# Kernel tuning notes

Hardware: AMD Instinct MI355X
Metric: run time of the kernel (lower is better)

Reference implementation:

```python
import jax, jax.numpy as jnp
import numpy as np
import math

INPUT_SIZE = 1024
OUTPUT_SIZE = 1024
N_HEADS = 8
N_EXPERTS = 16
PROJ = INPUT_SIZE // N_HEADS  # 128


def sinusoidal_pos_embedding(d_model, max_len, pos_offset):
    # positions pos_offset .. pos_offset+max_len-1, standard sin/cos interleave
    position = (jnp.arange(max_len, dtype=jnp.float32) + pos_offset)[:, None]
    div_term = jnp.exp(jnp.arange(0, d_model, 2, dtype=jnp.float32) * (-math.log(10000.0) / d_model))
    pe = jnp.zeros((max_len, d_model), dtype=jnp.float32)
    pe = pe.at[:, 0::2].set(jnp.sin(position * div_term))
    pe = pe.at[:, 1::2].set(jnp.cos(position * div_term))
    return pe


def shift(posmat):
    # Transformer-XL style relative shift: [..., n_out, 2*n_in-1] -> [..., n_out, n_in]
    n_in = (posmat.shape[-1] + 1) // 2
    n_neg = n_in - 1
    n_out = posmat.shape[-2]
    x = posmat.reshape(posmat.shape[:-2] + (-1,))
    x = x[..., 1:1 + n_out * (n_in + n_neg - 1)]
    x = x.reshape(x.shape[:-1] + (n_out, n_in + n_neg - 1))
    return x[..., n_neg - 1:]


def setup_inputs() -> dict:
    key = jax.random.key(0)
    ks = jax.random.split(key, 8)
    B, S = 4, 1024
    std_in = math.sqrt(1.0 / INPUT_SIZE)
    std_out = math.sqrt(1.0 / (N_HEADS * PROJ))
    std_pos = math.sqrt(1.0 / INPUT_SIZE)
    return {
        "curr_state": jax.random.normal(ks[0], (B, S, INPUT_SIZE), jnp.float32),
        "attend_to": jax.random.normal(ks[1], (B, S, INPUT_SIZE), jnp.float32),
        "data_to_q": jax.random.normal(ks[2], (N_EXPERTS, INPUT_SIZE, PROJ), jnp.float32) * std_in,
        "data_to_kv": jax.random.normal(ks[3], (INPUT_SIZE, 2 * PROJ), jnp.float32) * std_in,
        "out_proj": jax.random.normal(ks[4], (N_EXPERTS, PROJ, OUTPUT_SIZE), jnp.float32) * std_out,
        "pos_to_pk": jax.random.normal(ks[5], (PROJ, INPUT_SIZE), jnp.float32) * std_pos,
        "sel_dst": jax.random.normal(ks[6], (N_EXPERTS, INPUT_SIZE), jnp.float32) * std_in,
        "scale": jnp.full((1,), 1.0 / math.sqrt(PROJ), jnp.float32),
    }


def reference(curr_state, attend_to, data_to_q, data_to_kv, out_proj, pos_to_pk, sel_dst, scale):
    B, S, _ = curr_state.shape
    # --- expert selection (mode='my', sigmoid, eval: no expert dropout) ---
    sel = jnp.einsum('bsi,ei->bse', curr_state, sel_dst)           # gate logits
    sel_top, sel_index = jax.lax.top_k(sel, N_HEADS)               # [B,S,H]
    sel_val = jax.nn.sigmoid(sel_top)                              # [B,S,H]
    sc = jnp.sqrt(scale)                                           # scale applied to q, k, k_pos
    # --- relative position keys ---
    pemb = sinusoidal_pos_embedding(INPUT_SIZE, 2 * S - 1, -(S - 1))
    k_pos = (pemb @ pos_to_pk.T) * sc                              # [2S-1, P]
    # --- shared K/V ---
    kv = attend_to @ data_to_kv                                    # [B,S,2P]
    k = kv[..., :PROJ] * sc
    v = kv[..., PROJ:]
    # --- expert-selected Q (dense over experts, then gather selected) ---
    q_all = jnp.einsum('bsi,eip->bsep', curr_state, data_to_q) * sc  # [B,S,E,P]
    q = jnp.take_along_axis(q_all, sel_index[..., None], axis=2)     # [B,S,H,P]
    q = q.transpose(0, 2, 1, 3)                                      # [B,H,S,P]
    # --- attention with relative position shift (mask=None path) ---
    att = shift(jnp.einsum('bhsp,tp->bhst', q, k_pos)) + jnp.einsum('bhsp,btp->bhst', q, k)
    att = jax.nn.softmax(att, axis=-1)                               # [B,H,S,S]
    res = jnp.einsum('bhst,btp->bhsp', att, v)                       # [B,H,S,P]
    # --- expert-selected, sigmoid-gated output projection, summed over heads ---
    g = sel_val[..., None] * jax.nn.one_hot(sel_index, N_EXPERTS, dtype=res.dtype)  # [B,S,H,E]
    z = jnp.einsum('bshe,bhsp->bsep', g, res)                        # [B,S,E,P]
    out = jnp.einsum('bsep,epo->bso', z, out_proj)                   # [B,S,O]
    return out
```

## Files before the change

### kernel.cpp

```cpp
#include <hip/hip_runtime.h>
#include <math.h>


typedef __attribute__((ext_vector_type(8))) short short8;
typedef __attribute__((ext_vector_type(4))) float floatx4;

__device__ __forceinline__ float bf2f(unsigned int u) {
    union { unsigned int i; float f; } x; x.i = (u & 0xffffu) << 16; return x.f;
}
__device__ __forceinline__ unsigned short f2bf(float f) {
    union { float f; unsigned int i; } x; x.f = f;
    unsigned int r = x.i + 0x7fffu + ((x.i >> 16) & 1u);
    return (unsigned short)(r >> 16);
}

__device__ __forceinline__ void gload16(const void* g, void* l) {
    __builtin_amdgcn_global_load_lds(
        (const __attribute__((address_space(1))) unsigned int*)(uintptr_t)g,
        (__attribute__((address_space(3))) unsigned int*)(uintptr_t)l,
        16, 0, 0);
}


__global__ __launch_bounds__(256) void k_prep(const float* __restrict__ curr,
                                              const float* __restrict__ attend,
                                              const float* __restrict__ w_q,
                                              const float* __restrict__ w_out,
                                              const float* __restrict__ w_kv,
                                              const float* __restrict__ pos_pk,
                                              const float* __restrict__ sel_dst,
                                              float* __restrict__ selval,
                                              int* __restrict__ selidx,
                                              unsigned short* __restrict__ afrag,
                                              unsigned short* __restrict__ attfrag,
                                              unsigned short* __restrict__ bfragq,
                                              unsigned short* __restrict__ bfragw,
                                              unsigned short* __restrict__ bfragkv,
                                              unsigned short* __restrict__ bfragp,
                                              unsigned short* __restrict__ pefrag) {
    __shared__ float row[1024];
    __shared__ float sel[16];
    const int bx = blockIdx.x;
    const int t = threadIdx.x;

    if (bx < 2048) {
        const unsigned u = (unsigned)bx * 256 + t;
        const int half = u & 1;
        const int nlow = (u >> 1) & 15;
        const int koct = (u >> 5) & 3;
        const int kc   = (u >> 7) & 31;
        const int nt   = (u >> 12) & 127;
        const int n = nt * 16 + nlow;
        const int e = n >> 7, p = n & 127;
        const int k0 = kc * 32 + koct * 8 + half * 4;
        const float* src = w_q + (size_t)e * 131072 + (size_t)k0 * 128 + p;
        uint2 o;
        o.x = (unsigned)f2bf(src[0])   | ((unsigned)f2bf(src[128]) << 16);
        o.y = (unsigned)f2bf(src[256]) | ((unsigned)f2bf(src[384]) << 16);
        const size_t chunk = ((size_t)nt * 32 + kc) * 64 + koct * 16 + nlow;
        *(uint2*)(bfragq + chunk * 8 + half * 4) = o;
    } else if (bx < 4096) {
        const unsigned u = (unsigned)(bx - 2048) * 256 + t;
        const int half = u & 1;
        const int nlow = (u >> 1) & 15;
        const int koct = (u >> 5) & 3;
        const int kc   = (u >> 7) & 63;
        const int nt   = (u >> 13) & 63;
        const int n = nt * 16 + nlow;
        const int k0 = kc * 32 + koct * 8 + half * 4;
        const float* src = w_out + (size_t)k0 * 1024 + n;
        uint2 o;
        o.x = (unsigned)f2bf(src[0])    | ((unsigned)f2bf(src[1024]) << 16);
        o.y = (unsigned)f2bf(src[2048]) | ((unsigned)f2bf(src[3072]) << 16);
        const size_t chunk = ((size_t)nt * 64 + kc) * 64 + koct * 16 + nlow;
        *(uint2*)(bfragw + chunk * 8 + half * 4) = o;
    } else if (bx < 4352) {
        const unsigned u = (unsigned)(bx - 4096) * 256 + t;
        const int half = u & 1;
        const int nlow = (u >> 1) & 15;
        const int koct = (u >> 5) & 3;
        const int kc   = (u >> 7) & 31;
        const int nt   = (u >> 12) & 15;
        const int n = nt * 16 + nlow;
        const int k0 = kc * 32 + koct * 8 + half * 4;
        const float* src = w_kv + (size_t)k0 * 256 + n;
        uint2 o;
        o.x = (unsigned)f2bf(src[0])   | ((unsigned)f2bf(src[256]) << 16);
        o.y = (unsigned)f2bf(src[512]) | ((unsigned)f2bf(src[768]) << 16);
        const size_t chunk = ((size_t)nt * 32 + kc) * 64 + koct * 16 + nlow;
        *(uint2*)(bfragkv + chunk * 8 + half * 4) = o;
    } else if (bx < 4480) {
        const int n = bx - 4352;
        float v[4];
#pragma unroll
        for (int d = 0; d < 4; ++d) v[d] = pos_pk[(size_t)n * 1024 + 4 * t + d];
        const int nt = n >> 4, kc = t >> 3;
        const int lane = ((t & 7) >> 1) * 16 + (n & 15);
        const size_t off = (((size_t)nt * 32 + kc) * 64 + lane) * 8 + 4 * (t & 1);
        uint2 o;
        o.x = (unsigned)f2bf(v[0]) | ((unsigned)f2bf(v[1]) << 16);
        o.y = (unsigned)f2bf(v[2]) | ((unsigned)f2bf(v[3]) << 16);
        *(uint2*)(bfragp + off) = o;
    } else if (bx < 6528) {
        const unsigned u = (unsigned)(bx - 4480) * 256 + t;
        const int half = u & 1;
        const int mlow = (u >> 1) & 15;
        const int koct = (u >> 5) & 3;
        const int kc   = (u >> 7) & 31;
        const int mt   = (u >> 12) & 127;
        const int m = mt * 16 + mlow;
        const int k0 = kc * 32 + koct * 8 + half * 4;
        uint2 o;
        if (m >= 2047) {
            o.x = 0u; o.y = 0u;
        } else {
            const float c1 = -logf(10000.f) / 1024.f;
            const float pos = (float)(m - 1023);
            const float a0 = pos * expf((float)k0 * c1);
            const float a1 = pos * expf((float)(k0 + 2) * c1);
            o.x = (unsigned)f2bf(sinf(a0)) | ((unsigned)f2bf(cosf(a0)) << 16);
            o.y = (unsigned)f2bf(sinf(a1)) | ((unsigned)f2bf(cosf(a1)) << 16);
        }
        const size_t chunk = ((size_t)mt * 32 + kc) * 64 + koct * 16 + mlow;
        *(uint2*)(pefrag + chunk * 8 + half * 4) = o;
    } else if (bx < 10624) {
        const int token = bx - 6528;
        const float4 v = ((const float4*)(curr + (size_t)token * 1024))[t];
        ((float4*)row)[t] = v;
        __syncthreads();
        const int wv = t >> 6, lane = t & 63;
        for (int e0 = 0; e0 < 4; ++e0) {
            const int e = wv * 4 + e0;
            const float* w = sel_dst + e * 1024;
            float p = 0.f;
            for (int i = lane; i < 1024; i += 64) p += row[i] * w[i];
            for (int off = 32; off; off >>= 1) p += __shfl_down(p, off, 64);
            if (lane == 0) sel[e] = p;
        }
        __syncthreads();
        if (t == 0) {
            float v16[16];
#pragma unroll
            for (int e = 0; e < 16; ++e) v16[e] = sel[e];
#pragma unroll
            for (int r = 0; r < 8; ++r) {
                int bi = 0; float bv = v16[0];
#pragma unroll
                for (int e = 1; e < 16; ++e) { if (v16[e] > bv) { bv = v16[e]; bi = e; } }
                selidx[token * 8 + r] = bi;
                selval[token * 8 + r] = 1.f / (1.f + __expf(-bv));
                v16[bi] = -INFINITY;
            }
        }
    } else if (bx < 14720) {
        const unsigned u = (unsigned)(bx - 10624) * 256 + t;
        const int half = u & 1;
        const int mlow = (u >> 1) & 15;
        const int koct = (u >> 5) & 3;
        const int kc   = (u >> 7) & 31;
        const int mt   = (u >> 12) & 255;
        const int m = mt * 16 + mlow;
        const int k0 = kc * 32 + koct * 8 + half * 4;
        const float4 v = *(const float4*)(curr + (size_t)m * 1024 + k0);
        uint2 o;
        o.x = (unsigned)f2bf(v.x) | ((unsigned)f2bf(v.y) << 16);
        o.y = (unsigned)f2bf(v.z) | ((unsigned)f2bf(v.w) << 16);
        const size_t chunk = ((size_t)mt * 32 + kc) * 64 + koct * 16 + mlow;
        *(uint2*)(afrag + chunk * 8 + half * 4) = o;
    } else {
        const unsigned u = (unsigned)(bx - 14720) * 256 + t;
        const int half = u & 1;
        const int mlow = (u >> 1) & 15;
        const int koct = (u >> 5) & 3;
        const int kc   = (u >> 7) & 31;
        const int mt   = (u >> 12) & 255;
        const int m = mt * 16 + mlow;
        const int k0 = kc * 32 + koct * 8 + half * 4;
        const float4 v = *(const float4*)(attend + (size_t)m * 1024 + k0);
        uint2 o;
        o.x = (unsigned)f2bf(v.x) | ((unsigned)f2bf(v.y) << 16);
        o.y = (unsigned)f2bf(v.z) | ((unsigned)f2bf(v.w) << 16);
        const size_t chunk = ((size_t)mt * 32 + kc) * 64 + koct * 16 + mlow;
        *(uint2*)(attfrag + chunk * 8 + half * 4) = o;
    }
}

__device__ __forceinline__ void gemm_core64(const unsigned short* __restrict__ Afrag,
                                            const unsigned short* __restrict__ Bfrag,
                                            int mt0, int nt0, int KC,
                                            unsigned short (*aT)[512],
                                            unsigned short (*bT)[512],
                                            floatx4 acc[4][2]) {
    const int t = threadIdx.x;
    const int w = t >> 6, lane = t & 63;
    const int wm = w >> 1, wn = w & 1;
    for (int kc = 0; kc < KC; ++kc) {
        __syncthreads();
        {
            const int fi = w * 3;
#pragma unroll
            for (int l = 0; l < 3; ++l) {
                const int f = fi + l;
                if (f < 8)
                    gload16(Afrag + (((size_t)(mt0 + f) * KC + kc) * 64 + lane) * 8, &aT[f][0]);
                else
                    gload16(Bfrag + (((size_t)(nt0 + f - 8) * KC + kc) * 64 + lane) * 8, &bT[f - 8][0]);
            }
        }
        __syncthreads();
        short8 af[4], bf[2];
#pragma unroll
        for (int i = 0; i < 4; ++i) af[i] = *(const short8*)&aT[wm * 4 + i][lane * 8];
#pragma unroll
        for (int j = 0; j < 2; ++j) bf[j] = *(const short8*)&bT[wn * 2 + j][lane * 8];
#pragma unroll
        for (int i = 0; i < 4; ++i)
#pragma unroll
            for (int j = 0; j < 2; ++j)
                acc[i][j] = __builtin_amdgcn_mfma_f32_16x16x32_bf16(af[i], bf[j], acc[i][j], 0, 0, 0);
    }
}

__global__ __launch_bounds__(256) void k_gemm3(const unsigned short* __restrict__ afrag,
                                               const unsigned short* __restrict__ bfragq,
                                               const unsigned short* __restrict__ attfrag,
                                               const unsigned short* __restrict__ bfragkv,
                                               const unsigned short* __restrict__ pefrag,
                                               const unsigned short* __restrict__ bfragp,
                                               const float* __restrict__ scale,
                                               unsigned short* __restrict__ qall,
                                               unsigned short* __restrict__ kfragg,
                                               unsigned short* __restrict__ vfragg,
                                               unsigned short* __restrict__ kposfg) {
    __shared__ __align__(16) unsigned short aT[8][512], bT[4][512];
    floatx4 acc[4][2];
#pragma unroll
    for (int i = 0; i < 4; ++i) { acc[i][0] = (floatx4){0,0,0,0}; acc[i][1] = (floatx4){0,0,0,0}; }
    const int bx = blockIdx.x;
    const int t = threadIdx.x, w = t >> 6, lane = t & 63;
    const int wm = w >> 1, wn = w & 1, lq = lane >> 4, lm = lane & 15;
    const float sc = sqrtf(scale[0]);

    if (bx < 1024) {
        const int gx = bx & 31, gy = bx >> 5;
        gemm_core64(afrag, bfragq, gx * 8, gy * 4, 32, aT, bT, acc);
#pragma unroll
        for (int i = 0; i < 4; ++i)
#pragma unroll
            for (int j = 0; j < 2; ++j)
#pragma unroll
                for (int r = 0; r < 4; ++r)
                    qall[(size_t)(gx * 128 + (wm * 4 + i) * 16 + lq * 4 + r) * 2048 +
                         gy * 64 + (wn * 2 + j) * 16 + lm] = f2bf(acc[i][j][r] * sc);
    } else if (bx < 1152) {
        const int q = bx - 1024;
        const int gx = q & 31, gy = q >> 5;
        gemm_core64(attfrag, bfragkv, gx * 8, gy * 4, 32, aT, bT, acc);
#pragma unroll
        for (int i = 0; i < 4; ++i)
#pragma unroll
            for (int j = 0; j < 2; ++j) {
                const int n = gy * 64 + (wn * 2 + j) * 16 + lm;
#pragma unroll
                for (int r = 0; r < 4; ++r) {
                    const int tok = gx * 128 + (wm * 4 + i) * 16 + lq * 4 + r;
                    const int bb = tok >> 10, jj = tok & 1023;
                    if (n < 128) {
                        const int p = n;
                        const size_t addr = ((((size_t)bb * 64 + (jj >> 4)) * 4 + (p >> 5)) * 64 +
                                             ((p & 31) >> 3) * 16 + (jj & 15)) * 8 + (p & 7);
                        kfragg[addr] = f2bf(acc[i][j][r] * sc);
                    } else {
                        const int p = n - 128;
                        const size_t addr = ((((size_t)bb * 32 + (jj >> 5)) * 8 + (p >> 4)) * 64 +
                                             ((jj & 31) >> 3) * 16 + (p & 15)) * 8 + (jj & 7);
                        vfragg[addr] = f2bf(acc[i][j][r]);
                    }
                }
            }
    } else {
        const int q = bx - 1152;
        const int gx = q & 15, gy = q >> 4;
        gemm_core64(pefrag, bfragp, gx * 8, gy * 4, 32, aT, bT, acc);
#pragma unroll
        for (int i = 0; i < 4; ++i)
#pragma unroll
            for (int j = 0; j < 2; ++j) {
                const int p = gy * 64 + (wn * 2 + j) * 16 + lm;
#pragma unroll
                for (int r = 0; r < 4; ++r) {
                    const int tp = gx * 128 + (wm * 4 + i) * 16 + lq * 4 + r;
                    const size_t addr = (((size_t)(tp >> 4) * 4 + (p >> 5)) * 64 +
                                         ((p & 31) >> 3) * 16 + (tp & 15)) * 8 + (p & 7);
                    kposfg[addr] = f2bf(acc[i][j][r] * sc);
                }
            }
    }
}

__global__ __launch_bounds__(256) void k_gemm_out(const unsigned short* __restrict__ Afrag,
                                                  const unsigned short* __restrict__ Bfrag,
                                                  float* __restrict__ out) {
    __shared__ __align__(16) unsigned short aT[8][512], bT[4][512];
    floatx4 acc[4][2];
#pragma unroll
    for (int i = 0; i < 4; ++i) { acc[i][0] = (floatx4){0,0,0,0}; acc[i][1] = (floatx4){0,0,0,0}; }
    gemm_core64(Afrag, Bfrag, blockIdx.x * 8, blockIdx.y * 4, 64, aT, bT, acc);
    const int t = threadIdx.x, w = t >> 6, lane = t & 63;
    const int wm = w >> 1, wn = w & 1, lq = lane >> 4, lm = lane & 15;
#pragma unroll
    for (int i = 0; i < 4; ++i)
#pragma unroll
        for (int j = 0; j < 2; ++j)
#pragma unroll
            for (int r = 0; r < 4; ++r)
                out[(size_t)(blockIdx.x * 128 + (wm * 4 + i) * 16 + lq * 4 + r) * 1024 +
                    blockIdx.y * 64 + (wn * 2 + j) * 16 + lm] = acc[i][j][r];
}

#define ATTN_FM 8.0f

__global__ __launch_bounds__(256, 2) void k_attn(const unsigned short* __restrict__ qall,
                                                 const unsigned short* __restrict__ kfragg,
                                                 const unsigned short* __restrict__ vfragg,
                                                 const unsigned short* __restrict__ kposfg,
                                                 const int* __restrict__ selidx,
                                                 const float* __restrict__ selval,
                                                 unsigned short* __restrict__ zfrag) {
    __shared__ __align__(16) union {
        struct {
            unsigned short pl[2][4][16][56];
            unsigned short kst[2][2][8][512];
            unsigned short vst[2][2][8][512];
        } s;
        float cmb[2][64][37];
    } sh;

    const int t = threadIdx.x;
    const int w = t >> 6, lane = t & 63;
    const int st = blockIdx.x & 63;
    const int hg = (blockIdx.x >> 6) & 3;
    const int b = blockIdx.x >> 8;
    const int wh = w & 1;
    const int ws = w >> 1;
    const int h = hg * 2 + wh;
    const int s0 = st * 16;
    const int lq = lane >> 4;
    const int lm = lane & 15;
    const int loff = lane * 16;

    short8 qf[4];
    {
        const int token = b * 1024 + s0 + lm;
        const int e = selidx[token * 8 + h];
        const unsigned short* qb = qall + (size_t)token * 2048 + e * 128 + lq * 8;
#pragma unroll
        for (int c = 0; c < 4; ++c) qf[c] = *(const short8*)(qb + c * 32);
    }
    short8 onesf;
#pragma unroll
    for (int i = 0; i < 8; ++i) onesf[i] = (short)0x3F80;

    int baddr[4], bsel[4];
#pragma unroll
    for (int r = 0; r < 4; ++r) {
        const int c0 = 15 + lm - (lq * 4 + r);
        baddr[r] = (lq * 16 + (c0 & 15)) * 4;
        bsel[r] = (c0 < 16) ? 1 : 0;
    }

    floatx4 acc[8], accl;
#pragma unroll
    for (int nt = 0; nt < 8; ++nt) acc[nt] = (floatx4){0.f, 0.f, 0.f, 0.f};
    accl = (floatx4){0.f, 0.f, 0.f, 0.f};

    const size_t koff = (size_t)ws * 131072;
    const char* pk = (const char*)kfragg + (size_t)b * 262144 + koff;
    const char* pv = (const char*)vfragg + (size_t)b * 262144 + koff;
    const char* pp = (const char*)kposfg + (size_t)((1008 - s0) >> 4) * 4096 + koff;

    if (wh == 0) {
#pragma unroll
        for (int q = 0; q < 8; ++q)
            gload16(pk + q * 1024 + loff, &sh.s.kst[0][ws][q][0]);
    } else {
#pragma unroll
        for (int q = 0; q < 8; ++q)
            gload16(pv + q * 1024 + loff, &sh.s.vst[0][ws][q][0]);
    }
    short8 n1c[4], n2c[4];
    floatx4 sp_carry = {0.f, 0.f, 0.f, 0.f};
    {
        short8 cry[4];
#pragma unroll
        for (int c = 0; c < 4; ++c) {
            cry[c] = *(const short8*)(pp + c * 1024 + loff);
            n1c[c] = *(const short8*)(pp + 4096 + c * 1024 + loff);
            n2c[c] = *(const short8*)(pp + 8192 + c * 1024 + loff);
        }
#pragma unroll
        for (int c = 0; c < 4; ++c)
            sp_carry = __builtin_amdgcn_mfma_f32_16x16x32_bf16(qf[c], cry[c], sp_carry, 0, 0, 0);
    }
    __syncthreads();

    unsigned short* pl0 = &sh.s.pl[0][w][0][0];
    unsigned short* pl1 = &sh.s.pl[1][w][0][0];

    for (int it = 0; it < 16; ++it) {
        const int cur = it & 1, nxt = cur ^ 1;
        if (it < 15) {
            if (wh == 0) {
#pragma unroll
                for (int q = 0; q < 8; ++q)
                    gload16(pk + 8192 + q * 1024 + loff, &sh.s.kst[nxt][ws][q][0]);
            } else {
#pragma unroll
                for (int q = 0; q < 8; ++q)
                    gload16(pv + 8192 + q * 1024 + loff, &sh.s.vst[nxt][ws][q][0]);
            }
        }
        short8 n1n[4], n2n[4];
        if (it < 15) {
#pragma unroll
            for (int c = 0; c < 4; ++c) {
                n1n[c] = *(const short8*)(pp + 12288 + c * 1024 + loff);
                n2n[c] = *(const short8*)(pp + 16384 + c * 1024 + loff);
            }
        }
        const floatx4 sp0 = sp_carry;
        floatx4 sp1 = {0.f, 0.f, 0.f, 0.f}, sp2 = {0.f, 0.f, 0.f, 0.f};
#pragma unroll
        for (int c = 0; c < 4; ++c) {
            sp1 = __builtin_amdgcn_mfma_f32_16x16x32_bf16(qf[c], n1c[c], sp1, 0, 0, 0);
            sp2 = __builtin_amdgcn_mfma_f32_16x16x32_bf16(qf[c], n2c[c], sp2, 0, 0, 0);
        }
        floatx4 sk0 = {0.f, 0.f, 0.f, 0.f}, sk1 = {0.f, 0.f, 0.f, 0.f};
#pragma unroll
        for (int c = 0; c < 4; ++c) {
            const short8 k0 = *(const short8*)&sh.s.kst[cur][ws][c][lane * 8];
            const short8 k1 = *(const short8*)&sh.s.kst[cur][ws][4 + c][lane * 8];
            sk0 = __builtin_amdgcn_mfma_f32_16x16x32_bf16(qf[c], k0, sk0, 0, 0, 0);
            sk1 = __builtin_amdgcn_mfma_f32_16x16x32_bf16(qf[c], k1, sk1, 0, 0, 0);
        }
        unsigned short* pl = cur ? pl1 : pl0;
#pragma unroll
        for (int r = 0; r < 4; ++r) {
            const int a = baddr[r];
            const float b0 = __int_as_float(__builtin_amdgcn_ds_bpermute(a, __float_as_int(sp0[r])));
            const float b1 = __int_as_float(__builtin_amdgcn_ds_bpermute(a, __float_as_int(sp1[r])));
            const float b2 = __int_as_float(__builtin_amdgcn_ds_bpermute(a, __float_as_int(sp2[r])));
            const float v0 = sk0[r] + (bsel[r] ? b0 : b1);
            const float v1 = sk1[r] + (bsel[r] ? b1 : b2);
            pl[(lq * 4 + r) * 56 + lm]      = f2bf(__expf(v0 - ATTN_FM));
            pl[(lq * 4 + r) * 56 + 16 + lm] = f2bf(__expf(v1 - ATTN_FM));
        }
        asm volatile("" ::: "memory");
        const short8 pf = *(const short8*)(pl + lm * 56 + lq * 8);
#pragma unroll
        for (int nt = 0; nt < 8; ++nt) {
            const short8 vf = *(const short8*)&sh.s.vst[cur][ws][nt][lane * 8];
            acc[nt] = __builtin_amdgcn_mfma_f32_16x16x32_bf16(pf, vf, acc[nt], 0, 0, 0);
        }
        accl = __builtin_amdgcn_mfma_f32_16x16x32_bf16(pf, onesf, accl, 0, 0, 0);
        sp_carry = sp2;
#pragma unroll
        for (int c = 0; c < 4; ++c) { n1c[c] = n1n[c]; n2c[c] = n2n[c]; }
        pk += 8192; pv += 8192; pp += 8192;
        __syncthreads();
    }

    if (ws == 1) {
        float* cb = &sh.cmb[wh][lane][0];
#pragma unroll
        for (int nt = 0; nt < 8; ++nt)
#pragma unroll
            for (int r = 0; r < 4; ++r) cb[nt * 4 + r] = acc[nt][r];
#pragma unroll
        for (int r = 0; r < 4; ++r) cb[32 + r] = accl[r];
    }
    __syncthreads();
    if (ws == 1) return;
    {
        const float* cb = &sh.cmb[wh][lane][0];
#pragma unroll
        for (int nt = 0; nt < 8; ++nt)
#pragma unroll
            for (int r = 0; r < 4; ++r) acc[nt][r] += cb[nt * 4 + r];
#pragma unroll
        for (int r = 0; r < 4; ++r) accl[r] += cb[32 + r];
    }

#pragma unroll
    for (int r = 0; r < 4; ++r) {
        const int tok = b * 1024 + s0 + lq * 4 + r;
        const int e = selidx[tok * 8 + h];
        const float g = selval[tok * 8 + h] / accl[r];
        const int mt = tok >> 4, tm = tok & 15;
#pragma unroll
        for (int nt = 0; nt < 8; ++nt) {
            const int k = e * 128 + nt * 16 + lm;
            const int kc = k >> 5;
            const int lane2 = (((k & 31) >> 3) << 4) + tm;
            zfrag[(((size_t)mt * 64 + kc) * 64 + lane2) * 8 + (k & 7)] = f2bf(acc[nt][r] * g);
        }
    }
}

extern "C" void kernel_launch(void* const* d_in, const int* in_sizes, int n_in,
                              void* d_out, int out_size, void* d_ws, size_t ws_size,
                              hipStream_t stream) {
    const float* curr    = (const float*)d_in[0];
    const float* attend  = (const float*)d_in[1];
    const float* w_q     = (const float*)d_in[2];
    const float* w_kv    = (const float*)d_in[3];
    const float* w_out   = (const float*)d_in[4];
    const float* pos_pk  = (const float*)d_in[5];
    const float* sel_dst = (const float*)d_in[6];
    const float* scale   = (const float*)d_in[7];
    float* out = (float*)d_out;

    char* ws = (char*)d_ws;
    float* selval = (float*)ws;
    int*   selidx = (int*)(ws + 131072);
    unsigned short* kposfg  = (unsigned short*)(ws + 262144);
    unsigned short* kfragg  = (unsigned short*)(ws + 786432);
    unsigned short* vfragg  = (unsigned short*)(ws + 1835008);
    unsigned short* bfragq  = (unsigned short*)(ws + 2883584);
    unsigned short* bfragw  = (unsigned short*)(ws + 7077888);
    unsigned short* bfragkv = (unsigned short*)(ws + 11272192);
    unsigned short* afrag   = (unsigned short*)(ws + 11796480);
    unsigned short* qall    = (unsigned short*)(ws + 20185088);
    unsigned short* zfrag   = (unsigned short*)(ws + 36962304);
    unsigned short* pefrag  = zfrag;
    unsigned short* bfragp  = zfrag + 2097152;
    unsigned short* attfrag = zfrag + 4194304;

    k_prep<<<18816, 256, 0, stream>>>(curr, attend, w_q, w_out, w_kv, pos_pk, sel_dst,
                                      selval, selidx, afrag, attfrag,
                                      bfragq, bfragw, bfragkv, bfragp, pefrag);
    k_gemm3<<<1184, 256, 0, stream>>>(afrag, bfragq, attfrag, bfragkv, pefrag, bfragp,
                                      scale, qall, kfragg, vfragg, kposfg);
    hipMemsetAsync(zfrag, 0, (size_t)16777216, stream);
    k_attn<<<1024, 256, 0, stream>>>(qall, kfragg, vfragg, kposfg, selidx, selval, zfrag);
    k_gemm_out<<<dim3(32, 16), 256, 0, stream>>>(zfrag, bfragw, out);
}
```

Measured before the change: 270.3 us.

## Process two query tiles per attention wave to reuse K/V loads

```diff
diff --git a/kernel.cpp b/kernel.cpp
--- a/kernel.cpp
+++ b/kernel.cpp
@@ -329,33 +329,34 @@
                                                  unsigned short* __restrict__ zfrag) {
     __shared__ __align__(16) union {
         struct {
-            unsigned short pl[2][4][16][56];
-            unsigned short kst[2][2][8][512];
-            unsigned short vst[2][2][8][512];
+            unsigned short pl[4][2][16][56];
+            unsigned short kst[2][8][512];
+            unsigned short vst[2][8][512];
         } s;
-        float cmb[2][64][37];
+        float cmb[2][2][64][37];
     } sh;
 
     const int t = threadIdx.x;
     const int w = t >> 6, lane = t & 63;
-    const int st = blockIdx.x & 63;
-    const int hg = (blockIdx.x >> 6) & 3;
-    const int b = blockIdx.x >> 8;
+    const int st2 = blockIdx.x & 31;
+    const int hg = (blockIdx.x >> 5) & 3;
+    const int b = blockIdx.x >> 7;
     const int wh = w & 1;
     const int ws = w >> 1;
     const int h = hg * 2 + wh;
-    const int s0 = st * 16;
+    const int s0 = st2 * 32;
     const int lq = lane >> 4;
     const int lm = lane & 15;
     const int loff = lane * 16;
 
-    short8 qf[4];
-    {
-        const int token = b * 1024 + s0 + lm;
+    short8 qf[2][4];
+#pragma unroll
+    for (int qt = 0; qt < 2; ++qt) {
+        const int token = b * 1024 + s0 + qt * 16 + lm;
         const int e = selidx[token * 8 + h];
         const unsigned short* qb = qall + (size_t)token * 2048 + e * 128 + lq * 8;
 #pragma unroll
-        for (int c = 0; c < 4; ++c) qf[c] = *(const short8*)(qb + c * 32);
+        for (int c = 0; c < 4; ++c) qf[qt][c] = *(const short8*)(qb + c * 32);
     }
     short8 onesf;
 #pragma unroll
@@ -369,142 +370,139 @@
         bsel[r] = (c0 < 16) ? 1 : 0;
     }
 
-    floatx4 acc[8], accl;
-#pragma unroll
-    for (int nt = 0; nt < 8; ++nt) acc[nt] = (floatx4){0.f, 0.f, 0.f, 0.f};
-    accl = (floatx4){0.f, 0.f, 0.f, 0.f};
+    floatx4 acc[2][8], accl[2];
+#pragma unroll
+    for (int qt = 0; qt < 2; ++qt) {
+#pragma unroll
+        for (int nt = 0; nt < 8; ++nt) acc[qt][nt] = (floatx4){0.f, 0.f, 0.f, 0.f};
+        accl[qt] = (floatx4){0.f, 0.f, 0.f, 0.f};
+    }
 
     const size_t koff = (size_t)ws * 131072;
     const char* pk = (const char*)kfragg + (size_t)b * 262144 + koff;
     const char* pv = (const char*)vfragg + (size_t)b * 262144 + koff;
-    const char* pp = (const char*)kposfg + (size_t)((1008 - s0) >> 4) * 4096 + koff;
-
-    if (wh == 0) {
-#pragma unroll
-        for (int q = 0; q < 8; ++q)
-            gload16(pk + q * 1024 + loff, &sh.s.kst[0][ws][q][0]);
-    } else {
-#pragma unroll
-        for (int q = 0; q < 8; ++q)
-            gload16(pv + q * 1024 + loff, &sh.s.vst[0][ws][q][0]);
-    }
-    short8 n1c[4], n2c[4];
-    floatx4 sp_carry = {0.f, 0.f, 0.f, 0.f};
+    const char* pp = (const char*)kposfg + (size_t)(63 - 2 * st2) * 4096 + koff;
+
+    floatx4 spc[2] = {{0.f,0.f,0.f,0.f},{0.f,0.f,0.f,0.f}};
     {
-        short8 cry[4];
 #pragma unroll
         for (int c = 0; c < 4; ++c) {
-            cry[c] = *(const short8*)(pp + c * 1024 + loff);
-            n1c[c] = *(const short8*)(pp + 4096 + c * 1024 + loff);
-            n2c[c] = *(const short8*)(pp + 8192 + c * 1024 + loff);
-        }
-#pragma unroll
-        for (int c = 0; c < 4; ++c)
-            sp_carry = __builtin_amdgcn_mfma_f32_16x16x32_bf16(qf[c], cry[c], sp_carry, 0, 0, 0);
-    }
+            const short8 c0 = *(const short8*)(pp + c * 1024 + loff);
+            const short8 c1 = *(const short8*)(pp - 4096 + c * 1024 + loff);
+            spc[0] = __builtin_amdgcn_mfma_f32_16x16x32_bf16(qf[0][c], c0, spc[0], 0, 0, 0);
+            spc[1] = __builtin_amdgcn_mfma_f32_16x16x32_bf16(qf[1][c], c1, spc[1], 0, 0, 0);
+        }
+    }
+
+    unsigned short* plw[2] = { &sh.s.pl[w][0][0][0], &sh.s.pl[w][1][0][0] };
+
+    for (int it = 0; it < 16; ++it) {
+        __syncthreads();
+        if (wh == 0) {
+#pragma unroll
+            for (int q = 0; q < 8; ++q)
+                gload16(pk + q * 1024 + loff, &sh.s.kst[ws][q][0]);
+        } else {
+#pragma unroll
+            for (int q = 0; q < 8; ++q)
+                gload16(pv + q * 1024 + loff, &sh.s.vst[ws][q][0]);
+        }
+        floatx4 sp1[2] = {{0.f,0.f,0.f,0.f},{0.f,0.f,0.f,0.f}};
+        floatx4 sp2[2] = {{0.f,0.f,0.f,0.f},{0.f,0.f,0.f,0.f}};
+#pragma unroll
+        for (int c = 0; c < 4; ++c) {
+            const short8 ta = *(const short8*)(pp + c * 1024 + loff);
+            const short8 tb = *(const short8*)(pp + 4096 + c * 1024 + loff);
+            const short8 tc = *(const short8*)(pp + 8192 + c * 1024 + loff);
+            sp1[0] = __builtin_amdgcn_mfma_f32_16x16x32_bf16(qf[0][c], tb, sp1[0], 0, 0, 0);
+            sp2[0] = __builtin_amdgcn_mfma_f32_16x16x32_bf16(qf[0][c], tc, sp2[0], 0, 0, 0);
+            sp1[1] = __builtin_amdgcn_mfma_f32_16x16x32_bf16(qf[1][c], ta, sp1[1], 0, 0, 0);
+            sp2[1] = __builtin_amdgcn_mfma_f32_16x16x32_bf16(qf[1][c], tb, sp2[1], 0, 0, 0);
+        }
+        __syncthreads();
+        floatx4 sk0[2] = {{0.f,0.f,0.f,0.f},{0.f,0.f,0.f,0.f}};
+        floatx4 sk1[2] = {{0.f,0.f,0.f,0.f},{0.f,0.f,0.f,0.f}};
+#pragma unroll
+        for (int c = 0; c < 4; ++c) {
+            const short8 k0 = *(const short8*)&sh.s.kst[ws][c][lane * 8];
+            const short8 k1 = *(const short8*)&sh.s.kst[ws][4 + c][lane * 8];
+            sk0[0] = __builtin_amdgcn_mfma_f32_16x16x32_bf16(qf[0][c], k0, sk0[0], 0, 0, 0);
+            sk1[0] = __builtin_amdgcn_mfma_f32_16x16x32_bf16(qf[0][c], k1, sk1[0], 0, 0, 0);
+            sk0[1] = __builtin_amdgcn_mfma_f32_16x16x32_bf16(qf[1][c], k0, sk0[1], 0, 0, 0);
+            sk1[1] = __builtin_amdgcn_mfma_f32_16x16x32_bf16(qf[1][c], k1, sk1[1], 0, 0, 0);
+        }
+#pragma unroll
+        for (int qt = 0; qt < 2; ++qt) {
+            unsigned short* pl = plw[qt];
+#pragma unroll
+            for (int r = 0; r < 4; ++r) {
+                const int a = baddr[r];
+                const float b0 = __int_as_float(__builtin_amdgcn_ds_bpermute(a, __float_as_int(spc[qt][r])));
+                const float b1 = __int_as_float(__builtin_amdgcn_ds_bpermute(a, __float_as_int(sp1[qt][r])));
+                const float b2 = __int_as_float(__builtin_amdgcn_ds_bpermute(a, __float_as_int(sp2[qt][r])));
+                const float v0 = sk0[qt][r] + (bsel[r] ? b0 : b1);
+                const float v1 = sk1[qt][r] + (bsel[r] ? b1 : b2);
+                pl[(lq * 4 + r) * 56 + lm]      = f2bf(__expf(v0 - ATTN_FM));
+                pl[(lq * 4 + r) * 56 + 16 + lm] = f2bf(__expf(v1 - ATTN_FM));
+            }
+        }
+        asm volatile("" ::: "memory");
+        const short8 pf0 = *(const short8*)(plw[0] + lm * 56 + lq * 8);
+        const short8 pf1 = *(const short8*)(plw[1] + lm * 56 + lq * 8);
+#pragma unroll
+        for (int nt = 0; nt < 8; ++nt) {
+            const short8 vf = *(const short8*)&sh.s.vst[ws][nt][lane * 8];
+            acc[0][nt] = __builtin_amdgcn_mfma_f32_16x16x32_bf16(pf0, vf, acc[0][nt], 0, 0, 0);
+            acc[1][nt] = __builtin_amdgcn_mfma_f32_16x16x32_bf16(pf1, vf, acc[1][nt], 0, 0, 0);
+        }
+        accl[0] = __builtin_amdgcn_mfma_f32_16x16x32_bf16(pf0, onesf, accl[0], 0, 0, 0);
+        accl[1] = __builtin_amdgcn_mfma_f32_16x16x32_bf16(pf1, onesf, accl[1], 0, 0, 0);
+        spc[0] = sp2[0]; spc[1] = sp2[1];
+        pk += 8192; pv += 8192; pp += 8192;
+    }
+
     __syncthreads();
-
-    unsigned short* pl0 = &sh.s.pl[0][w][0][0];
-    unsigned short* pl1 = &sh.s.pl[1][w][0][0];
-
-    for (int it = 0; it < 16; ++it) {
-        const int cur = it & 1, nxt = cur ^ 1;
-        if (it < 15) {
-            if (wh == 0) {
-#pragma unroll
-                for (int q = 0; q < 8; ++q)
-                    gload16(pk + 8192 + q * 1024 + loff, &sh.s.kst[nxt][ws][q][0]);
-            } else {
-#pragma unroll
-                for (int q = 0; q < 8; ++q)
-                    gload16(pv + 8192 + q * 1024 + loff, &sh.s.vst[nxt][ws][q][0]);
-            }
-        }
-        short8 n1n[4], n2n[4];
-        if (it < 15) {
-#pragma unroll
-            for (int c = 0; c < 4; ++c) {
-                n1n[c] = *(const short8*)(pp + 12288 + c * 1024 + loff);
-                n2n[c] = *(const short8*)(pp + 16384 + c * 1024 + loff);
-            }
-        }
-        const floatx4 sp0 = sp_carry;
-        floatx4 sp1 = {0.f, 0.f, 0.f, 0.f}, sp2 = {0.f, 0.f, 0.f, 0.f};
-#pragma unroll
-        for (int c = 0; c < 4; ++c) {
-            sp1 = __builtin_amdgcn_mfma_f32_16x16x32_bf16(qf[c], n1c[c], sp1, 0, 0, 0);
-            sp2 = __builtin_amdgcn_mfma_f32_16x16x32_bf16(qf[c], n2c[c], sp2, 0, 0, 0);
-        }
-        floatx4 sk0 = {0.f, 0.f, 0.f, 0.f}, sk1 = {0.f, 0.f, 0.f, 0.f};
-#pragma unroll
-        for (int c = 0; c < 4; ++c) {
-            const short8 k0 = *(const short8*)&sh.s.kst[cur][ws][c][lane * 8];
-            const short8 k1 = *(const short8*)&sh.s.kst[cur][ws][4 + c][lane * 8];
-            sk0 = __builtin_amdgcn_mfma_f32_16x16x32_bf16(qf[c], k0, sk0, 0, 0, 0);
-            sk1 = __builtin_amdgcn_mfma_f32_16x16x32_bf16(qf[c], k1, sk1, 0, 0, 0);
-        }
-        unsigned short* pl = cur ? pl1 : pl0;
-#pragma unroll
-        for (int r = 0; r < 4; ++r) {
-            const int a = baddr[r];
-            const float b0 = __int_as_float(__builtin_amdgcn_ds_bpermute(a, __float_as_int(sp0[r])));
-            const float b1 = __int_as_float(__builtin_amdgcn_ds_bpermute(a, __float_as_int(sp1[r])));
-            const float b2 = __int_as_float(__builtin_amdgcn_ds_bpermute(a, __float_as_int(sp2[r])));
-            const float v0 = sk0[r] + (bsel[r] ? b0 : b1);
-            const float v1 = sk1[r] + (bsel[r] ? b1 : b2);
-            pl[(lq * 4 + r) * 56 + lm]      = f2bf(__expf(v0 - ATTN_FM));
-            pl[(lq * 4 + r) * 56 + 16 + lm] = f2bf(__expf(v1 - ATTN_FM));
-        }
-        asm volatile("" ::: "memory");
-        const short8 pf = *(const short8*)(pl + lm * 56 + lq * 8);
-#pragma unroll
-        for (int nt = 0; nt < 8; ++nt) {
-            const short8 vf = *(const short8*)&sh.s.vst[cur][ws][nt][lane * 8];
-            acc[nt] = __builtin_amdgcn_mfma_f32_16x16x32_bf16(pf, vf, acc[nt], 0, 0, 0);
-        }
-        accl = __builtin_amdgcn_mfma_f32_16x16x32_bf16(pf, onesf, accl, 0, 0, 0);
-        sp_carry = sp2;
-#pragma unroll
-        for (int c = 0; c < 4; ++c) { n1c[c] = n1n[c]; n2c[c] = n2n[c]; }
-        pk += 8192; pv += 8192; pp += 8192;
-        __syncthreads();
-    }
-
     if (ws == 1) {
-        float* cb = &sh.cmb[wh][lane][0];
-#pragma unroll
-        for (int nt = 0; nt < 8; ++nt)
-#pragma unroll
-            for (int r = 0; r < 4; ++r) cb[nt * 4 + r] = acc[nt][r];
-#pragma unroll
-        for (int r = 0; r < 4; ++r) cb[32 + r] = accl[r];
+#pragma unroll
+        for (int qt = 0; qt < 2; ++qt) {
+            float* cb = &sh.cmb[wh][qt][lane][0];
+#pragma unroll
+            for (int nt = 0; nt < 8; ++nt)
+#pragma unroll
+                for (int r = 0; r < 4; ++r) cb[nt * 4 + r] = acc[qt][nt][r];
+#pragma unroll
+            for (int r = 0; r < 4; ++r) cb[32 + r] = accl[qt][r];
+        }
     }
     __syncthreads();
     if (ws == 1) return;
-    {
-        const float* cb = &sh.cmb[wh][lane][0];
+#pragma unroll
+    for (int qt = 0; qt < 2; ++qt) {
+        const float* cb = &sh.cmb[wh][qt][lane][0];
 #pragma unroll
         for (int nt = 0; nt < 8; ++nt)
 #pragma unroll
-            for (int r = 0; r < 4; ++r) acc[nt][r] += cb[nt * 4 + r];
-#pragma unroll
-        for (int r = 0; r < 4; ++r) accl[r] += cb[32 + r];
-    }
-
-#pragma unroll
-    for (int r = 0; r < 4; ++r) {
-        const int tok = b * 1024 + s0 + lq * 4 + r;
-        const int e = selidx[tok * 8 + h];
-        const float g = selval[tok * 8 + h] / accl[r];
-        const int mt = tok >> 4, tm = tok & 15;
-#pragma unroll
-        for (int nt = 0; nt < 8; ++nt) {
-            const int k = e * 128 + nt * 16 + lm;
-            const int kc = k >> 5;
-            const int lane2 = (((k & 31) >> 3) << 4) + tm;
-            zfrag[(((size_t)mt * 64 + kc) * 64 + lane2) * 8 + (k & 7)] = f2bf(acc[nt][r] * g);
-        }
-    }
+            for (int r = 0; r < 4; ++r) acc[qt][nt][r] += cb[nt * 4 + r];
+#pragma unroll
+        for (int r = 0; r < 4; ++r) accl[qt][r] += cb[32 + r];
+    }
+
+#pragma unroll
+    for (int qt = 0; qt < 2; ++qt)
+#pragma unroll
+        for (int r = 0; r < 4; ++r) {
+            const int tok = b * 1024 + s0 + qt * 16 + lq * 4 + r;
+            const int e = selidx[tok * 8 + h];
+            const float g = selval[tok * 8 + h] / accl[qt][r];
+            const int mt = tok >> 4, tm = tok & 15;
+#pragma unroll
+            for (int nt = 0; nt < 8; ++nt) {
+                const int k = e * 128 + nt * 16 + lm;
+                const int kc = k >> 5;
+                const int lane2 = (((k & 31) >> 3) << 4) + tm;
+                zfrag[(((size_t)mt * 64 + kc) * 64 + lane2) * 8 + (k & 7)] = f2bf(acc[qt][nt][r] * g);
+            }
+        }
 }
 
 extern "C" void kernel_launch(void* const* d_in, const int* in_sizes, int n_in,
@@ -542,6 +540,6 @@
     k_gemm3<<<1184, 256, 0, stream>>>(afrag, bfragq, attfrag, bfragkv, pefrag, bfragp,
                                       scale, qall, kfragg, vfragg, kposfg);
     hipMemsetAsync(zfrag, 0, (size_t)16777216, stream);
-    k_attn<<<1024, 256, 0, stream>>>(qall, kfragg, vfragg, kposfg, selidx, selval, zfrag);
+    k_attn<<<512, 256, 0, stream>>>(qall, kfragg, vfragg, kposfg, selidx, selval, zfrag);
     k_gemm_out<<<dim3(32, 16), 256, 0, stream>>>(zfrag, bfragw, out);
 }
```

New measurement: 259.4 us. 4.0% less time.
